# Performance work log

Measured on AMD Instinct MI355X. Metric: run time of the kernel, lower is better.

The kernel has to match this reference:

```python
import jax, jax.numpy as jnp
import numpy as np
from jax import lax

V, E, H, K = 50000, 128, 256, 9
B, T = 64, 512


def setup_inputs() -> dict:
    key = jax.random.key(0)
    ks = jax.random.split(key, 16)
    s = 0.05
    return {
        "x": jax.random.randint(ks[0], (B, T), 0, V),
        "tags": jax.random.randint(ks[1], (B, T), 0, K),
        "mask": jnp.ones((B, T), dtype=bool),
        "embed_table": jax.random.normal(ks[2], (V, E), jnp.float32) * s,
        "w_ih_f": jax.random.normal(ks[3], (4 * H, E), jnp.float32) * s,
        "w_hh_f": jax.random.normal(ks[4], (4 * H, H), jnp.float32) * s,
        "b_ih_f": jax.random.normal(ks[5], (4 * H,), jnp.float32) * s,
        "b_hh_f": jax.random.normal(ks[6], (4 * H,), jnp.float32) * s,
        "w_ih_b": jax.random.normal(ks[7], (4 * H, E), jnp.float32) * s,
        "w_hh_b": jax.random.normal(ks[8], (4 * H, H), jnp.float32) * s,
        "b_ih_b": jax.random.normal(ks[9], (4 * H,), jnp.float32) * s,
        "b_hh_b": jax.random.normal(ks[10], (4 * H,), jnp.float32) * s,
        "w_tag": jax.random.normal(ks[11], (K, 2 * H), jnp.float32) * s,
        "b_tag": jax.random.normal(ks[12], (K,), jnp.float32) * s,
        "start_trans": jax.random.normal(ks[13], (K,), jnp.float32) * s,
        "end_trans": jax.random.normal(ks[14], (K,), jnp.float32) * s,
        "trans": jax.random.normal(ks[15], (K, K), jnp.float32) * s,
    }


def _lstm_dir(x_tbe, w_ih, w_hh, b_ih, b_hh, reverse=False):
    # x_tbe: [T, B, E]; torch gate order: i, f, g, o
    h0 = jnp.zeros((x_tbe.shape[1], H), x_tbe.dtype)
    c0 = jnp.zeros_like(h0)
    xg = jnp.einsum('tbe,ge->tbg', x_tbe, w_ih) + b_ih + b_hh  # precompute input gates

    def step(carry, xg_t):
        h, c = carry
        g = xg_t + h @ w_hh.T
        i, f, gg, o = jnp.split(g, 4, axis=-1)
        c = jax.nn.sigmoid(f) * c + jax.nn.sigmoid(i) * jnp.tanh(gg)
        h = jax.nn.sigmoid(o) * jnp.tanh(c)
        return (h, c), h

    _, hs = lax.scan(step, (h0, c0), xg, reverse=reverse)
    return hs  # [T, B, H]


def _crf_nll(emissions, tags, mask, start_trans, end_trans, trans):
    # emissions: [B,T,K]; tags: [B,T] int; mask: [B,T] bool. torchcrf, reduction='sum'.
    Bc, Tc, Kc = emissions.shape
    maskf = mask.astype(emissions.dtype)
    barange = jnp.arange(Bc)
    # numerator: score of gold path
    em_scores = jnp.take_along_axis(emissions, tags[..., None], axis=-1)[..., 0]  # [B,T]
    trans_scores = trans[tags[:, :-1], tags[:, 1:]]  # [B,T-1]
    num = start_trans[tags[:, 0]] + em_scores[:, 0]
    num = num + jnp.sum((em_scores[:, 1:] + trans_scores) * maskf[:, 1:], axis=1)
    last_idx = (jnp.sum(maskf, axis=1) - 1).astype(jnp.int32)
    last_tags = tags[barange, last_idx]
    num = num + end_trans[last_tags]
    # denominator: forward algorithm (log partition)
    alpha0 = start_trans[None, :] + emissions[:, 0]  # [B,K]

    def step(alpha, inp):
        em_t, m_t = inp  # [B,K], [B]
        nxt = jax.nn.logsumexp(alpha[:, :, None] + trans[None] + em_t[:, None, :], axis=1)
        return jnp.where(m_t[:, None], nxt, alpha), None

    alpha, _ = lax.scan(step, alpha0,
                        (jnp.swapaxes(emissions[:, 1:], 0, 1), mask[:, 1:].T))
    denom = jax.nn.logsumexp(alpha + end_trans[None, :], axis=1)
    llh = jnp.sum(num - denom)  # reduction='sum'
    return -llh


def reference(x, tags, mask, embed_table,
              w_ih_f, w_hh_f, b_ih_f, b_hh_f,
              w_ih_b, w_hh_b, b_ih_b, b_hh_b,
              w_tag, b_tag, start_trans, end_trans, trans):
    embedded = embed_table[x]                     # [B,T,E]
    x_tbe = jnp.swapaxes(embedded, 0, 1)          # [T,B,E]
    h_f = _lstm_dir(x_tbe, w_ih_f, w_hh_f, b_ih_f, b_hh_f, reverse=False)
    h_b = _lstm_dir(x_tbe, w_ih_b, w_hh_b, b_ih_b, b_hh_b, reverse=True)
    lstm_out = jnp.concatenate([h_f, h_b], axis=-1)         # [T,B,2H]
    lstm_out = jnp.swapaxes(lstm_out, 0, 1)                 # [B,T,2H]
    emissions = jnp.einsum('btd,kd->btk', lstm_out, w_tag) + b_tag
    return _crf_nll(emissions, tags, mask, start_trans, end_trans, trans)
```

## Files before the change

kernel.cpp:

```cpp
#include <hip/hip_runtime.h>
#include <stdint.h>


#define TT 512
#define BB 64
#define EE 128
#define HH 256

typedef __attribute__((ext_vector_type(8))) short short8;
typedef __attribute__((ext_vector_type(4))) float floatx4;
typedef __attribute__((ext_vector_type(2))) float floatx2;
typedef __attribute__((ext_vector_type(4))) unsigned uintx4;
typedef __attribute__((ext_vector_type(8))) unsigned uintx8;

__device__ __forceinline__ unsigned short f2bf(float f) {
    union { float f; unsigned u; } c; c.f = f;
    return (unsigned short)((c.u + 0x7FFFu + ((c.u >> 16) & 1u)) >> 16);
}
__device__ __forceinline__ unsigned pk_fp8x4(float a, float b, float c, float d) {
    int v = __builtin_amdgcn_cvt_pk_fp8_f32(a, b, 0, false);
    v = __builtin_amdgcn_cvt_pk_fp8_f32(c, d, v, true);
    return (unsigned)v;
}

__global__ __launch_bounds__(256)
void prep_kernel(const float* __restrict__ whf, const float* __restrict__ whb,
                 const float* __restrict__ wihf, const float* __restrict__ wihb,
                 unsigned* __restrict__ wre, unsigned short* __restrict__ wih_bf)
{
    const int bid = blockIdx.x, tid = threadIdx.x;
    if (bid < 512) {
        int idx = bid * 256 + tid;
        int j4   = idx & 7;
        int gcb  = (idx >> 3) & 7;
        int lane = (idx >> 6) & 63;
        int K0   = (idx >> 12) & 1;
        int wv   = (idx >> 13) & 7;
        int dir  = idx >> 16;
        int g = gcb >> 1, cb = gcb & 1;
        int l15 = lane & 15, lh = lane >> 4;
        int grow = g * 256 + wv * 32 + cb * 16 + l15;
        int k0 = K0 * 128 + lh * 32 + j4 * 4;
        const float* w = dir ? whb : whf;
        const float4 v = *(const float4*)(w + (size_t)grow * HH + k0);
        wre[idx] = pk_fp8x4(v.x, v.y, v.z, v.w);
    } else {
        int idx = (bid - 512) * 256 + tid;
        int dir = idx >> 14, rem = idx & 16383;
        const float* w = dir ? wihb : wihf;
        const float* s = w + (size_t)rem * 8;
        short8 v;
        #pragma unroll
        for (int j = 0; j < 8; ++j) v[j] = (short)f2bf(s[j]);
        *(short8*)(wih_bf + (size_t)idx * 8) = v;
    }
}

__global__ __launch_bounds__(256, 2)
void xg_kernel(const int* __restrict__ x, const float* __restrict__ embed,
               const unsigned short* __restrict__ wih_bf,
               const float* __restrict__ b_ih_f, const float* __restrict__ b_hh_f,
               const float* __restrict__ b_ih_b, const float* __restrict__ b_hh_b,
               unsigned* __restrict__ xg2)
{
    const int bid = blockIdx.x;
    const int dir = bid >> 10, t4 = (bid >> 3) & 127, nt = bid & 7;
    const int tid = threadIdx.x, lane = tid & 63, wv = tid >> 6;
    const int l15 = lane & 15, lh = lane >> 4;
    const float* b_ih = dir ? b_ih_b : b_ih_f;
    const float* b_hh = dir ? b_hh_b : b_hh_f;

    __shared__ int xid[64];
    __shared__ __align__(16) unsigned short As[64][136];
    __shared__ __align__(16) unsigned char Fs[64][144];
    __shared__ float bsh[128];

    if (tid < 128) bsh[tid] = b_ih[nt * 128 + tid] + b_hh[nt * 128 + tid];

    short8 wfr[8][4];
    const unsigned short* wbase = wih_bf + (size_t)dir * 131072;
    #pragma unroll
    for (int mt = 0; mt < 8; ++mt) {
        int grow = nt * 128 + mt * 16 + l15;
        #pragma unroll
        for (int kt = 0; kt < 4; ++kt)
            wfr[mt][kt] = *(const short8*)(wbase + (size_t)grow * EE + kt * 32 + lh * 8);
    }

    for (int tt = 0; tt < 4; ++tt) {
        const int t = t4 * 4 + tt;
        __syncthreads();
        if (tid < 64) xid[tid] = x[tid * TT + t];
        __syncthreads();
        for (int i = tid; i < 2048; i += 256) {
            int b = i >> 5, seg = i & 31;
            float4 v = *(const float4*)(embed + (size_t)xid[b] * EE + seg * 4);
            union { unsigned short u[4]; unsigned long long q; } p;
            p.u[0] = f2bf(v.x); p.u[1] = f2bf(v.y); p.u[2] = f2bf(v.z); p.u[3] = f2bf(v.w);
            *(unsigned long long*)&As[b][seg * 4] = p.q;
        }
        __syncthreads();

        floatx4 acc[8];
        #pragma unroll
        for (int mt = 0; mt < 8; ++mt) acc[mt] = (floatx4){0.f, 0.f, 0.f, 0.f};
        #pragma unroll
        for (int kt = 0; kt < 4; ++kt) {
            short8 af = *(const short8*)&As[wv * 16 + l15][kt * 32 + lh * 8];
            #pragma unroll
            for (int mt = 0; mt < 8; ++mt)
                acc[mt] = __builtin_amdgcn_mfma_f32_16x16x32_bf16(wfr[mt][kt], af, acc[mt], 0, 0, 0);
        }
        #pragma unroll
        for (int mt = 0; mt < 8; ++mt) {
            int j0 = mt * 16 + lh * 4;
            unsigned u = pk_fp8x4(acc[mt][0] + bsh[j0], acc[mt][1] + bsh[j0 + 1],
                                  acc[mt][2] + bsh[j0 + 2], acc[mt][3] + bsh[j0 + 3]);
            *(unsigned*)&Fs[wv * 16 + l15][j0] = u;
        }
        __syncthreads();
        for (int i = tid; i < 2048; i += 256) {
            int b = i >> 5, jq = i & 31;
            unsigned v = *(const unsigned*)&Fs[b][jq * 4];
            int growq = nt * 128 + jq * 4;
            int g = growq >> 8, hcol4 = (growq & 255) >> 2;
            size_t o32 = (((size_t)(dir * TT + t) * 64 + b) * 4 + g) * 64 + hcol4;
            xg2[o32] = v;
        }
    }
}

#define WWPAIR(A0, A1, V)                                                     \
    asm volatile("v_accvgpr_write_b32 a" #A0 ", %0\n\t"                       \
                 "v_accvgpr_write_b32 a" #A1 ", %1"                           \
                 :: "v"((unsigned)(V)), "v"((unsigned)((V) >> 32))            \
                 : "a" #A0, "a" #A1)

#define MFMA128(N0, N7, ACC, HF)                                              \
    asm volatile("v_mfma_f32_16x16x128_f8f6f4 %0, a[" #N0 ":" #N7 "], %1, %0" \
                 : "+v"(ACC) : "v"(HF))

__global__ void __launch_bounds__(512)
__attribute__((amdgpu_waves_per_eu(2, 2)))
rec_kernel(const unsigned char* __restrict__ wre, const unsigned* __restrict__ xg2,
           unsigned* __restrict__ hout)
{
    const int dir = blockIdx.x & 1;
    const int bg  = blockIdx.x >> 1;
    const int tid = threadIdx.x, lane = tid & 63, wv = tid >> 6;
    const int l15 = lane & 15, lh = lane >> 4;
    const int bbase = bg * 4;

    __shared__ __align__(16) unsigned char hbuf[2][16][272];
    __shared__ __align__(16) float gseg[4 * 4 * 268];
    for (int i = tid; i < 2176; i += 512) ((int*)hbuf)[i] = 0;

    const unsigned char* wb = wre + (size_t)dir * 262144 + wv * 32768 + lane * 256;
    {
        ulonglong2 q0, q1;
#define LOADSLOT(OFF)                                                         \
        q0 = *(const ulonglong2*)(wb + (OFF));                                \
        q1 = *(const ulonglong2*)(wb + (OFF) + 16);
        LOADSLOT(0)     WWPAIR(0,1,q0.x);   WWPAIR(2,3,q0.y);   WWPAIR(4,5,q1.x);   WWPAIR(6,7,q1.y);
        LOADSLOT(32)    WWPAIR(8,9,q0.x);   WWPAIR(10,11,q0.y); WWPAIR(12,13,q1.x); WWPAIR(14,15,q1.y);
        LOADSLOT(64)    WWPAIR(16,17,q0.x); WWPAIR(18,19,q0.y); WWPAIR(20,21,q1.x); WWPAIR(22,23,q1.y);
        LOADSLOT(96)    WWPAIR(24,25,q0.x); WWPAIR(26,27,q0.y); WWPAIR(28,29,q1.x); WWPAIR(30,31,q1.y);
        LOADSLOT(128)   WWPAIR(32,33,q0.x); WWPAIR(34,35,q0.y); WWPAIR(36,37,q1.x); WWPAIR(38,39,q1.y);
        LOADSLOT(160)   WWPAIR(40,41,q0.x); WWPAIR(42,43,q0.y); WWPAIR(44,45,q1.x); WWPAIR(46,47,q1.y);
        LOADSLOT(192)   WWPAIR(48,49,q0.x); WWPAIR(50,51,q0.y); WWPAIR(52,53,q1.x); WWPAIR(54,55,q1.y);
        LOADSLOT(224)   WWPAIR(56,57,q0.x); WWPAIR(58,59,q0.y); WWPAIR(60,61,q1.x); WWPAIR(62,63,q1.y);
        LOADSLOT(16384) WWPAIR(64,65,q0.x); WWPAIR(66,67,q0.y); WWPAIR(68,69,q1.x); WWPAIR(70,71,q1.y);
        LOADSLOT(16416) WWPAIR(72,73,q0.x); WWPAIR(74,75,q0.y); WWPAIR(76,77,q1.x); WWPAIR(78,79,q1.y);
        LOADSLOT(16448) WWPAIR(80,81,q0.x); WWPAIR(82,83,q0.y); WWPAIR(84,85,q1.x); WWPAIR(86,87,q1.y);
        LOADSLOT(16480) WWPAIR(88,89,q0.x); WWPAIR(90,91,q0.y); WWPAIR(92,93,q1.x); WWPAIR(94,95,q1.y);
        LOADSLOT(16512) WWPAIR(96,97,q0.x);   WWPAIR(98,99,q0.y);   WWPAIR(100,101,q1.x); WWPAIR(102,103,q1.y);
        LOADSLOT(16544) WWPAIR(104,105,q0.x); WWPAIR(106,107,q0.y); WWPAIR(108,109,q1.x); WWPAIR(110,111,q1.y);
        LOADSLOT(16576) WWPAIR(112,113,q0.x); WWPAIR(114,115,q0.y); WWPAIR(116,117,q1.x); WWPAIR(118,119,q1.y);
        LOADSLOT(16608) WWPAIR(120,121,q0.x); WWPAIR(122,123,q0.y); WWPAIR(124,125,q1.x); WWPAIR(126,127,q1.y);
#undef LOADSLOT
    }

    float c[2] = {0.f, 0.f};

    const int eb = tid >> 7;
    const int ec2 = tid & 127;

    const unsigned char* xrb = (const unsigned char*)xg2
        + (size_t)(dir * TT + (dir ? TT - 1 : 0)) * 65536
        + (bbase + eb) * 1024 + ec2 * 2;
    const int xstep = dir ? -65536 : 65536;
    unsigned char* hdst = (unsigned char*)hout
        + ((size_t)(dir * TT + (dir ? TT - 1 : 0)) * BB + bbase + eb) * 256 + ec2 * 2;
    const int hstep = dir ? -16384 : 16384;

    const unsigned char* hbr = &hbuf[0][0][0];
    unsigned char* hbw = (unsigned char*)&hbuf[1][0][0];

    __syncthreads();

    for (int t = 0; t < TT; ++t) {
        unsigned short xs0 = *(const unsigned short*)(xrb);
        unsigned short xs1 = *(const unsigned short*)(xrb + 256);
        unsigned short xs2 = *(const unsigned short*)(xrb + 512);
        unsigned short xs3 = *(const unsigned short*)(xrb + 768);

        floatx4 acc[4][2];
        #pragma unroll
        for (int g = 0; g < 4; ++g)
            #pragma unroll
            for (int cb = 0; cb < 2; ++cb)
                acc[g][cb] = (floatx4){0.f, 0.f, 0.f, 0.f};
        asm volatile("s_nop 1");

        {
            const unsigned char* hrow = hbr + l15 * 272 + lh * 32;
            uintx8 hf0, hf1;
            ((uintx4*)&hf0)[0] = *(const uintx4*)(hrow);
            ((uintx4*)&hf0)[1] = *(const uintx4*)(hrow + 16);
            ((uintx4*)&hf1)[0] = *(const uintx4*)(hrow + 128);
            ((uintx4*)&hf1)[1] = *(const uintx4*)(hrow + 144);
            MFMA128(0,7,      acc[0][0], hf0); MFMA128(16,23,    acc[1][0], hf0);
            MFMA128(32,39,    acc[2][0], hf0); MFMA128(48,55,    acc[3][0], hf0);
            MFMA128(64,71,    acc[0][0], hf1); MFMA128(80,87,    acc[1][0], hf1);
            MFMA128(96,103,   acc[2][0], hf1); MFMA128(112,119,  acc[3][0], hf1);
            MFMA128(8,15,     acc[0][1], hf0); MFMA128(24,31,    acc[1][1], hf0);
            MFMA128(40,47,    acc[2][1], hf0); MFMA128(56,63,    acc[3][1], hf0);
            MFMA128(72,79,    acc[0][1], hf1); MFMA128(88,95,    acc[1][1], hf1);
            MFMA128(104,111,  acc[2][1], hf1); MFMA128(120,127,  acc[3][1], hf1);
        }
        asm volatile("s_nop 7\n\ts_nop 7\n\ts_nop 7\n\ts_nop 3");

        if (l15 < 4) {
            #pragma unroll
            for (int g = 0; g < 4; ++g) {
                float* gw = &gseg[(g * 4 + l15) * 268 + wv * 32 + lh * 4];
                *(floatx4*)(gw)      = acc[g][0];
                *(floatx4*)(gw + 16) = acc[g][1];
            }
        }
        __syncthreads();

        floatx2 gv0 = *(const floatx2*)&gseg[(0 * 4 + eb) * 268 + ec2 * 2];
        floatx2 gv1 = *(const floatx2*)&gseg[(1 * 4 + eb) * 268 + ec2 * 2];
        floatx2 gv2 = *(const floatx2*)&gseg[(2 * 4 + eb) * 268 + ec2 * 2];
        floatx2 gv3 = *(const floatx2*)&gseg[(3 * 4 + eb) * 268 + ec2 * 2];
        floatx2 xi_ = __builtin_amdgcn_cvt_pk_f32_fp8((int)(unsigned)xs0, false);
        floatx2 xf_ = __builtin_amdgcn_cvt_pk_f32_fp8((int)(unsigned)xs1, false);
        floatx2 xg_ = __builtin_amdgcn_cvt_pk_f32_fp8((int)(unsigned)xs2, false);
        floatx2 xo_ = __builtin_amdgcn_cvt_pk_f32_fp8((int)(unsigned)xs3, false);
        float hv2[2];
        #pragma unroll
        for (int r = 0; r < 2; ++r) {
            float iv = gv0[r] + xi_[r];
            float fv = gv1[r] + xf_[r];
            float gv = gv2[r] + xg_[r];
            float ov = gv3[r] + xo_[r];
            float A  = __expf(-iv);
            float C2 = __expf(-fv);
            float B  = __expf(-2.f * gv);
            float E  = __expf(-ov);
            float s1 = 1.f + A, s2 = 1.f + B, s3 = 1.f + C2, s4 = 1.f - B;
            float m1   = s1 * s2;
            float nsum = __builtin_fmaf(s4, s3, c[r] * m1);
            float den  = s3 * m1;
            float cv   = nsum * __builtin_amdgcn_rcpf(den);
            c[r] = cv;
            float F  = __expf(-2.f * cv);
            float s5 = 1.f + E, s6 = 1.f + F, s7 = 1.f - F;
            hv2[r] = s7 * __builtin_amdgcn_rcpf(s5 * s6);
        }
        unsigned short hp8 = (unsigned short)
            ((unsigned)__builtin_amdgcn_cvt_pk_fp8_f32(hv2[0], hv2[1], 0, false) & 0xFFFFu);
        *(unsigned short*)(hbw + eb * 272 + ec2 * 2) = hp8;
        __syncthreads();

        *(unsigned short*)hdst = hp8;
        hdst += hstep;
        xrb += xstep;
        { const unsigned char* tmp = hbr; hbr = hbw; hbw = (unsigned char*)tmp; }
    }
}

__global__ __launch_bounds__(256)
void em_kernel(const unsigned* __restrict__ hout, const float* __restrict__ w_tag,
               const float* __restrict__ b_tag, float* __restrict__ em)
{
    const int bid = blockIdx.x;
    const int b = bid >> 2, tq = bid & 3;
    const int tid = threadIdx.x, lane = tid & 63, wv = tid >> 6;
    const int dsel = lane >> 5, dloc = (lane & 31) * 8;

    float w72[9][8];
    #pragma unroll
    for (int k = 0; k < 9; ++k) {
        const float* src = w_tag + k * 512 + dsel * 256 + dloc;
        float4 a = *(const float4*)src;
        float4 b4 = *(const float4*)(src + 4);
        w72[k][0] = a.x;  w72[k][1] = a.y;  w72[k][2] = a.z;  w72[k][3] = a.w;
        w72[k][4] = b4.x; w72[k][5] = b4.y; w72[k][6] = b4.z; w72[k][7] = b4.w;
    }
    float btg = (lane < 9) ? b_tag[lane] : 0.f;

    for (int tt = wv; tt < 128; tt += 4) {
        int t = tq * 128 + tt;
        const unsigned* hp = hout + ((size_t)(dsel * TT + t) * BB + b) * 64 + (lane & 31) * 2;
        unsigned u0 = hp[0], u1 = hp[1];
        float hf[8];
        { floatx2 a = __builtin_amdgcn_cvt_pk_f32_fp8((int)u0, false);
          floatx2 b2 = __builtin_amdgcn_cvt_pk_f32_fp8((int)u0, true);
          hf[0]=a[0]; hf[1]=a[1]; hf[2]=b2[0]; hf[3]=b2[1]; }
        { floatx2 a = __builtin_amdgcn_cvt_pk_f32_fp8((int)u1, false);
          floatx2 b2 = __builtin_amdgcn_cvt_pk_f32_fp8((int)u1, true);
          hf[4]=a[0]; hf[5]=a[1]; hf[6]=b2[0]; hf[7]=b2[1]; }
        float p[9];
        #pragma unroll
        for (int k = 0; k < 9; ++k) {
            float s = 0.f;
            #pragma unroll
            for (int j = 0; j < 8; ++j) s += hf[j] * w72[k][j];
            p[k] = s;
        }
        float res = 0.f;
        #pragma unroll
        for (int k = 0; k < 9; ++k) {
            float s = p[k];
            s += __shfl_xor(s, 1);  s += __shfl_xor(s, 2);  s += __shfl_xor(s, 4);
            s += __shfl_xor(s, 8);  s += __shfl_xor(s, 16); s += __shfl_xor(s, 32);
            if (lane == k) res = s;
        }
        if (lane < 9) em[((size_t)b * TT + t) * 9 + lane] = res + btg;
    }
}

__global__ __launch_bounds__(256)
void scan_kernel(const float* __restrict__ em, const int* __restrict__ tags,
                 const float* __restrict__ st, const float* __restrict__ et,
                 const float* __restrict__ tr, float* __restrict__ out)
{
    const int b = blockIdx.x, tid = threadIdx.x;
    __shared__ float ems[4608];
    __shared__ float red[256];
    for (int i = tid; i < 4608; i += 256) ems[i] = em[(size_t)b * 4608 + i];
    __syncthreads();

    float nacc = 0.f;
    for (int t = tid; t < TT; t += 256) {
        int tg = tags[b * TT + t];
        float v = ems[t * 9 + tg];
        if (t > 0) v += tr[tags[b * TT + t - 1] * 9 + tg];
        nacc += v;
    }
    red[tid] = nacc;
    __syncthreads();
    for (int s = 128; s > 0; s >>= 1) {
        if (tid < s) red[tid] += red[tid + s];
        __syncthreads();
    }
    float num = red[0] + st[tags[b * TT]] + et[tags[b * TT + TT - 1]];

    if (tid < 64) {
        int kp = tid;
        int kpe = kp < 9 ? kp : 8;
        float trr[9];
        #pragma unroll
        for (int k = 0; k < 9; ++k) trr[k] = tr[k * 9 + kpe];
        float alpha = st[kpe] + ems[kpe];
        for (int t = 1; t < TT; ++t) {
            float av[9], m = -1e30f;
            #pragma unroll
            for (int k = 0; k < 9; ++k) { av[k] = __shfl(alpha, k) + trr[k]; m = fmaxf(m, av[k]); }
            float ssum = 0.f;
            #pragma unroll
            for (int k = 0; k < 9; ++k) ssum += __expf(av[k] - m);
            alpha = ems[t * 9 + kpe] + m + __logf(ssum);
        }
        float v = (kp < 9) ? (alpha + et[kpe]) : -1e30f;
        float m = v;
        m = fmaxf(m, __shfl_xor(m, 1));
        m = fmaxf(m, __shfl_xor(m, 2));
        m = fmaxf(m, __shfl_xor(m, 4));
        m = fmaxf(m, __shfl_xor(m, 8));
        float s = (kp < 9) ? __expf(v - m) : 0.f;
        s += __shfl_xor(s, 1);
        s += __shfl_xor(s, 2);
        s += __shfl_xor(s, 4);
        s += __shfl_xor(s, 8);
        if (kp == 0) atomicAdd(out, (m + __logf(s)) - num);
    }
}

extern "C" void kernel_launch(void* const* d_in, const int* in_sizes, int n_in,
                              void* d_out, int out_size, void* d_ws, size_t ws_size,
                              hipStream_t stream) {
    (void)in_sizes; (void)n_in; (void)out_size; (void)ws_size;
    const int* x        = (const int*)d_in[0];
    const int* tags     = (const int*)d_in[1];
    const float* embed  = (const float*)d_in[3];
    const float* w_ih_f = (const float*)d_in[4];
    const float* w_hh_f = (const float*)d_in[5];
    const float* b_ih_f = (const float*)d_in[6];
    const float* b_hh_f = (const float*)d_in[7];
    const float* w_ih_b = (const float*)d_in[8];
    const float* w_hh_b = (const float*)d_in[9];
    const float* b_ih_b = (const float*)d_in[10];
    const float* b_hh_b = (const float*)d_in[11];
    const float* w_tag  = (const float*)d_in[12];
    const float* b_tag  = (const float*)d_in[13];
    const float* st     = (const float*)d_in[14];
    const float* et     = (const float*)d_in[15];
    const float* tr     = (const float*)d_in[16];

    unsigned*       wre    = (unsigned*)d_ws;
    unsigned short* wih_bf = (unsigned short*)((char*)d_ws + 524288);
    unsigned*       xg2    = (unsigned*)((char*)d_ws + 1048576);
    unsigned*       hh     = (unsigned*)((char*)d_ws + 1048576 + 67108864);
    float*          em     = (float*)d_ws;

    hipMemsetAsync(d_out, 0, sizeof(float), stream);
    hipLaunchKernelGGL(prep_kernel, dim3(640), dim3(256), 0, stream,
                       w_hh_f, w_hh_b, w_ih_f, w_ih_b, wre, wih_bf);
    hipLaunchKernelGGL(xg_kernel, dim3(2048), dim3(256), 0, stream,
                       x, embed, wih_bf, b_ih_f, b_hh_f, b_ih_b, b_hh_b, xg2);
    hipLaunchKernelGGL(rec_kernel, dim3(32), dim3(512), 0, stream,
                       (const unsigned char*)wre, xg2, hh);
    hipLaunchKernelGGL(em_kernel, dim3(256), dim3(256), 0, stream,
                       hh, w_tag, b_tag, em);
    hipLaunchKernelGGL(scan_kernel, dim3(64), dim3(256), 0, stream,
                       em, tags, st, et, tr, (float*)d_out);
}
```

Before: 851.1 us.

## Split recurrent kernel across twice as many blocks with two batch rows each

The LSTM recurrence kernel now assigns two batch rows per block instead of four, doubling the grid from 32 to 64 blocks. Each thread handles one hidden unit instead of two, which halves the per-step elementwise gate work on the serial critical path. In exchange the MFMA work per step stays the same while fewer of its rows are useful, and each block still loads the full recurrent weights into registers, so total weight loading doubles.

```diff
diff --git a/kernel.cpp b/kernel.cpp
--- a/kernel.cpp
+++ b/kernel.cpp
@@ -149,10 +149,10 @@
     const int bg  = blockIdx.x >> 1;
     const int tid = threadIdx.x, lane = tid & 63, wv = tid >> 6;
     const int l15 = lane & 15, lh = lane >> 4;
-    const int bbase = bg * 4;
+    const int bbase = bg * 2;
 
     __shared__ __align__(16) unsigned char hbuf[2][16][272];
-    __shared__ __align__(16) float gseg[4 * 4 * 268];
+    __shared__ __align__(16) float gseg[4 * 2 * 268];
     for (int i = tid; i < 2176; i += 512) ((int*)hbuf)[i] = 0;
 
     const unsigned char* wb = wre + (size_t)dir * 262144 + wv * 32768 + lane * 256;
@@ -180,17 +180,17 @@
 #undef LOADSLOT
     }
 
-    float c[2] = {0.f, 0.f};
-
-    const int eb = tid >> 7;
-    const int ec2 = tid & 127;
+    float c = 0.f;
+
+    const int eb = tid >> 8;
+    const int ec = tid & 255;
 
     const unsigned char* xrb = (const unsigned char*)xg2
         + (size_t)(dir * TT + (dir ? TT - 1 : 0)) * 65536
-        + (bbase + eb) * 1024 + ec2 * 2;
+        + (bbase + eb) * 1024 + ec;
     const int xstep = dir ? -65536 : 65536;
     unsigned char* hdst = (unsigned char*)hout
-        + ((size_t)(dir * TT + (dir ? TT - 1 : 0)) * BB + bbase + eb) * 256 + ec2 * 2;
+        + ((size_t)(dir * TT + (dir ? TT - 1 : 0)) * BB + bbase + eb) * 256 + ec;
     const int hstep = dir ? -16384 : 16384;
 
     const unsigned char* hbr = &hbuf[0][0][0];
@@ -199,10 +199,7 @@
     __syncthreads();
 
     for (int t = 0; t < TT; ++t) {
-        unsigned short xs0 = *(const unsigned short*)(xrb);
-        unsigned short xs1 = *(const unsigned short*)(xrb + 256);
-        unsigned short xs2 = *(const unsigned short*)(xrb + 512);
-        unsigned short xs3 = *(const unsigned short*)(xrb + 768);
+        unsigned char xs0 = xrb[0], xs1 = xrb[256], xs2 = xrb[512], xs3 = xrb[768];
 
         floatx4 acc[4][2];
         #pragma unroll
@@ -230,51 +227,47 @@
         }
         asm volatile("s_nop 7\n\ts_nop 7\n\ts_nop 7\n\ts_nop 3");
 
-        if (l15 < 4) {
+        if (l15 < 2) {
             #pragma unroll
             for (int g = 0; g < 4; ++g) {
-                float* gw = &gseg[(g * 4 + l15) * 268 + wv * 32 + lh * 4];
+                float* gw = &gseg[(g * 2 + l15) * 268 + wv * 32 + lh * 4];
                 *(floatx4*)(gw)      = acc[g][0];
                 *(floatx4*)(gw + 16) = acc[g][1];
             }
         }
         __syncthreads();
 
-        floatx2 gv0 = *(const floatx2*)&gseg[(0 * 4 + eb) * 268 + ec2 * 2];
-        floatx2 gv1 = *(const floatx2*)&gseg[(1 * 4 + eb) * 268 + ec2 * 2];
-        floatx2 gv2 = *(const floatx2*)&gseg[(2 * 4 + eb) * 268 + ec2 * 2];
-        floatx2 gv3 = *(const floatx2*)&gseg[(3 * 4 + eb) * 268 + ec2 * 2];
-        floatx2 xi_ = __builtin_amdgcn_cvt_pk_f32_fp8((int)(unsigned)xs0, false);
-        floatx2 xf_ = __builtin_amdgcn_cvt_pk_f32_fp8((int)(unsigned)xs1, false);
-        floatx2 xg_ = __builtin_amdgcn_cvt_pk_f32_fp8((int)(unsigned)xs2, false);
-        floatx2 xo_ = __builtin_amdgcn_cvt_pk_f32_fp8((int)(unsigned)xs3, false);
-        float hv2[2];
-        #pragma unroll
-        for (int r = 0; r < 2; ++r) {
-            float iv = gv0[r] + xi_[r];
-            float fv = gv1[r] + xf_[r];
-            float gv = gv2[r] + xg_[r];
-            float ov = gv3[r] + xo_[r];
-            float A  = __expf(-iv);
-            float C2 = __expf(-fv);
-            float B  = __expf(-2.f * gv);
-            float E  = __expf(-ov);
-            float s1 = 1.f + A, s2 = 1.f + B, s3 = 1.f + C2, s4 = 1.f - B;
-            float m1   = s1 * s2;
-            float nsum = __builtin_fmaf(s4, s3, c[r] * m1);
-            float den  = s3 * m1;
-            float cv   = nsum * __builtin_amdgcn_rcpf(den);
-            c[r] = cv;
-            float F  = __expf(-2.f * cv);
-            float s5 = 1.f + E, s6 = 1.f + F, s7 = 1.f - F;
-            hv2[r] = s7 * __builtin_amdgcn_rcpf(s5 * s6);
-        }
-        unsigned short hp8 = (unsigned short)
-            ((unsigned)__builtin_amdgcn_cvt_pk_fp8_f32(hv2[0], hv2[1], 0, false) & 0xFFFFu);
-        *(unsigned short*)(hbw + eb * 272 + ec2 * 2) = hp8;
-        __syncthreads();
-
-        *(unsigned short*)hdst = hp8;
+        float gv0 = gseg[(0 * 2 + eb) * 268 + ec];
+        float gv1 = gseg[(1 * 2 + eb) * 268 + ec];
+        float gv2 = gseg[(2 * 2 + eb) * 268 + ec];
+        float gv3 = gseg[(3 * 2 + eb) * 268 + ec];
+        floatx2 xi2 = __builtin_amdgcn_cvt_pk_f32_fp8((int)(unsigned)xs0, false);
+        floatx2 xf2 = __builtin_amdgcn_cvt_pk_f32_fp8((int)(unsigned)xs1, false);
+        floatx2 xg2v = __builtin_amdgcn_cvt_pk_f32_fp8((int)(unsigned)xs2, false);
+        floatx2 xo2 = __builtin_amdgcn_cvt_pk_f32_fp8((int)(unsigned)xs3, false);
+        float iv = gv0 + xi2[0];
+        float fv = gv1 + xf2[0];
+        float gv = gv2 + xg2v[0];
+        float ov = gv3 + xo2[0];
+        float A  = __expf(-iv);
+        float C2 = __expf(-fv);
+        float B  = __expf(-2.f * gv);
+        float E  = __expf(-ov);
+        float s1 = 1.f + A, s2 = 1.f + B, s3 = 1.f + C2, s4 = 1.f - B;
+        float m1   = s1 * s2;
+        float nsum = __builtin_fmaf(s4, s3, c * m1);
+        float den  = s3 * m1;
+        float cv   = nsum * __builtin_amdgcn_rcpf(den);
+        c = cv;
+        float F  = __expf(-2.f * cv);
+        float s5 = 1.f + E, s6 = 1.f + F, s7 = 1.f - F;
+        float hv = s7 * __builtin_amdgcn_rcpf(s5 * s6);
+        unsigned char h8 = (unsigned char)
+            ((unsigned)__builtin_amdgcn_cvt_pk_fp8_f32(hv, hv, 0, false) & 0xFFu);
+        hbw[eb * 272 + ec] = h8;
+        __syncthreads();
+
+        *hdst = h8;
         hdst += hstep;
         xrb += xstep;
         { const unsigned char* tmp = hbr; hbr = hbw; hbw = (unsigned char*)tmp; }
@@ -421,7 +414,7 @@
                        w_hh_f, w_hh_b, w_ih_f, w_ih_b, wre, wih_bf);
     hipLaunchKernelGGL(xg_kernel, dim3(2048), dim3(256), 0, stream,
                        x, embed, wih_bf, b_ih_f, b_hh_f, b_ih_b, b_hh_b, xg2);
-    hipLaunchKernelGGL(rec_kernel, dim3(32), dim3(512), 0, stream,
+    hipLaunchKernelGGL(rec_kernel, dim3(64), dim3(512), 0, stream,
                        (const unsigned char*)wre, xg2, hh);
     hipLaunchKernelGGL(em_kernel, dim3(256), dim3(256), 0, stream,
                        hh, w_tag, b_tag, em);
```

Result: faster. 798.8 us (-6.2%).
